# Kernel tuning notes

Measured on AMD Instinct MI355X. Metric: run time of the kernel, lower is better.

Reference implementation:

```python
import jax, jax.numpy as jnp
import numpy as np

S, L, D = 512, 128, 256        # sents, sent_len, embedding_dim (= out_hidden, skip_rnn)
V, E_V, E_D = 50000, 10000, 64  # vocab, entity vocab, entity dim
B, P = 128, 16                  # batch examples, positions per example
H2, F = D // 2, 256             # attn hidden, feature_size


def setup_inputs() -> dict:
    key = jax.random.key(0)
    ks = jax.random.split(key, 16)
    emb = jax.random.normal(ks[0], (V, D), jnp.float32) * 0.02
    emb = emb.at[0].set(0.0)  # padding_idx=0
    ent_emb = jax.random.normal(ks[1], (E_V, E_D), jnp.float32) * 0.02
    ent_emb = ent_emb.at[0].set(0.0)
    x = jax.random.randint(ks[2], (S, L), 0, V)
    ents = jax.random.randint(ks[3], (B, 2), 0, E_V)
    spos = jax.random.randint(ks[4], (B, P, 2), 0, L)  # valid for both sent(<S) and tok(<L) axes
    tpos = jax.random.randint(ks[5], (B, P, 2), 0, L)
    attw_W = jax.random.normal(ks[6], (H2, D), jnp.float32) / np.sqrt(D)
    attw_b = jnp.zeros((H2,), jnp.float32)
    attw2_W = jax.random.normal(ks[7], (1, H2), jnp.float32) / np.sqrt(H2)
    FEAT = 2 * D + 2 * E_D
    cond_W = jax.random.normal(ks[8], (F, FEAT), jnp.float32) / np.sqrt(FEAT)
    cond_b = jnp.zeros((F,), jnp.float32)
    lin_W = jax.random.normal(ks[9], (2, F), jnp.float32) / np.sqrt(F)
    lin_b = jnp.zeros((2,), jnp.float32)
    return {"x": x, "ents": ents, "spos": spos, "tpos": tpos,
            "emb": emb, "ent_emb": ent_emb,
            "attw_W": attw_W, "attw_b": attw_b, "attw2_W": attw2_W,
            "cond_W": cond_W, "cond_b": cond_b, "lin_W": lin_W, "lin_b": lin_b}


def _attn_pool(h, attw_W, attw_b, attw2_W):
    # h: [B, P, D]  ->  [B, D]
    energy = jnp.tanh(jnp.einsum('bpd,hd->bph', h, attw_W) + attw_b)
    logits = jnp.einsum('bph,oh->bpo', energy, attw2_W)[..., 0]   # [B, P]
    w = jax.nn.softmax(logits, axis=1)
    return jnp.einsum('bp,bpd->bd', w, h)


def reference(x, ents, spos, tpos, emb, ent_emb, attw_W, attw_b, attw2_W,
              cond_W, cond_b, lin_W, lin_b):
    sent_hiddens = emb[x]                                  # [S, L, D] (skip_rnn path)
    s_h = sent_hiddens[spos[..., 0], spos[..., 1]]         # [B, P, D] ragged gather (batched)
    t_h = sent_hiddens[tpos[..., 0], tpos[..., 1]]         # [B, P, D]
    s_pool = _attn_pool(s_h, attw_W, attw_b, attw2_W)      # [B, D]
    t_pool = _attn_pool(t_h, attw_W, attw_b, attw2_W)      # [B, D]
    e_embs = ent_emb[ents].reshape(ents.shape[0], -1)      # [B, 2*E_D]
    feats = jnp.concatenate([s_pool, t_pool, e_embs], axis=-1)  # [B, 2D+2E_D]
    condensed = feats @ cond_W.T + cond_b                  # [B, F]
    score = jnp.tanh(condensed) @ lin_W.T + lin_b          # [B, 2]
    return score
```

## Files before the change

kernel.cpp:

```cpp
#include <hip/hip_runtime.h>

#define S_ 512
#define L_ 128
#define D_ 256
#define B_ 128
#define P_ 16
#define H2_ 128
#define F_ 256
#define FEAT_ 640
#define ED_ 64
#define SH_STRIDE 264
#define LP_STRIDE 33

__global__ __launch_bounds__(512) void fused_kernel(
    const int* __restrict__ x, const int* __restrict__ ents,
    const int* __restrict__ spos, const int* __restrict__ tpos,
    const float* __restrict__ emb, const float* __restrict__ ent_emb,
    const float* __restrict__ attw_W, const float* __restrict__ attw_b,
    const float* __restrict__ attw2_W,
    const float* __restrict__ cond_W, const float* __restrict__ cond_b,
    const float* __restrict__ lin_W, const float* __restrict__ lin_b,
    float* __restrict__ out)
{
    const int b = blockIdx.x;
    const int t = threadIdx.x;
    const int pool = t >> 8;
    const int tl = t & 255;

    __shared__ float sh[2 * P_ * SH_STRIDE];
    __shared__ float lp[2 * P_ * LP_STRIDE];
    __shared__ float logits[32];
    __shared__ float wts[32];
    __shared__ float feats[FEAT_];
    __shared__ float part0[F_], part1[F_];
    __shared__ float r0s[4], r1s[4];

    const int pool_off = pool * P_ * SH_STRIDE;

    {
        const int* pos = pool ? tpos : spos;
        const int p = tl >> 4, i = tl & 15;
        const int si  = pos[(b * P_ + p) * 2 + 0];
        const int ti  = pos[(b * P_ + p) * 2 + 1];
        const int tok = x[si * L_ + ti];
        const float4* row = (const float4*)(emb + (size_t)tok * D_);
        float4* dst = (float4*)&sh[pool_off + p * SH_STRIDE + i * 16];
        #pragma unroll
        for (int j = 0; j < 4; ++j) dst[j] = row[i * 4 + j];
    }
    __syncthreads();

    {
        const int hp = tl >> 3, dh = tl & 7;
        const int h0 = hp * 4;
        const float4* W4 = (const float4*)attw_W;
        float bq0 = attw_b[h0],     bq1 = attw_b[h0 + 1];
        float bq2 = attw_b[h0 + 2], bq3 = attw_b[h0 + 3];
        float wq0 = attw2_W[h0],     wq1 = attw2_W[h0 + 1];
        float wq2 = attw2_W[h0 + 2], wq3 = attw2_W[h0 + 3];

        #pragma unroll
        for (int pass = 0; pass < 2; ++pass) {
            const int pb = pass * 8;
            float acc[4][8];
            #pragma unroll
            for (int q = 0; q < 4; ++q)
                #pragma unroll
                for (int p = 0; p < 8; ++p) acc[q][p] = 0.f;

            float4 nxt[4];
            #pragma unroll
            for (int q = 0; q < 4; ++q) nxt[q] = W4[(h0 + q) * 64 + dh];

            for (int c = 0; c < 8; ++c) {
                float4 a[4];
                #pragma unroll
                for (int q = 0; q < 4; ++q) a[q] = nxt[q];
                if (c < 7) {
                    #pragma unroll
                    for (int q = 0; q < 4; ++q)
                        nxt[q] = W4[(h0 + q) * 64 + 8 * (c + 1) + dh];
                }
                const int d = (8 * c + dh) * 4;
                #pragma unroll
                for (int p = 0; p < 8; ++p) {
                    float4 s = *(const float4*)&sh[pool_off + (pb + p) * SH_STRIDE + d];
                    #pragma unroll
                    for (int q = 0; q < 4; ++q)
                        acc[q][p] += a[q].x * s.x + a[q].y * s.y + a[q].z * s.z + a[q].w * s.w;
                }
            }

            #pragma unroll
            for (int q = 0; q < 4; ++q) {
                #pragma unroll
                for (int j = 0; j < 4; ++j) {
                    float lo = acc[q][j],     olo = __shfl_xor(lo, 4, 64);
                    float hi = acc[q][j + 4], ohi = __shfl_xor(hi, 4, 64);
                    acc[q][j] = (dh & 4) ? (hi + ohi) : (lo + olo);
                }
                #pragma unroll
                for (int j = 0; j < 2; ++j) {
                    float lo = acc[q][j],     olo = __shfl_xor(lo, 2, 64);
                    float hi = acc[q][j + 2], ohi = __shfl_xor(hi, 2, 64);
                    acc[q][j] = (dh & 2) ? (hi + ohi) : (lo + olo);
                }
                {
                    float lo = acc[q][0], olo = __shfl_xor(lo, 1, 64);
                    float hi = acc[q][1], ohi = __shfl_xor(hi, 1, 64);
                    acc[q][0] = (dh & 1) ? (hi + ohi) : (lo + olo);
                }
            }
            float v = tanhf(acc[0][0] + bq0) * wq0 + tanhf(acc[1][0] + bq1) * wq1
                    + tanhf(acc[2][0] + bq2) * wq2 + tanhf(acc[3][0] + bq3) * wq3;
            lp[pool * P_ * LP_STRIDE + (pb + dh) * LP_STRIDE + hp] = v;
        }
    }
    __syncthreads();

    {
        const int p = tl >> 4, g = tl & 15;
        const float* l = &lp[pool * P_ * LP_STRIDE + p * LP_STRIDE];
        float s = l[2 * g] + l[2 * g + 1];
        #pragma unroll
        for (int m = 1; m <= 8; m <<= 1) s += __shfl_xor(s, m, 64);
        if (g == 0) logits[pool * 16 + p] = s;
    }
    __syncthreads();

    if (tl < 16) {
        float l = logits[pool * 16 + tl];
        float m = l;
        for (int mm = 8; mm >= 1; mm >>= 1) m = fmaxf(m, __shfl_xor(m, mm, 64));
        float e = expf(l - m);
        float ssum = e;
        for (int mm = 8; mm >= 1; mm >>= 1) ssum += __shfl_xor(ssum, mm, 64);
        wts[pool * 16 + tl] = e / ssum;
    }
    __syncthreads();

    {
        float acc = 0.f;
        #pragma unroll
        for (int p = 0; p < P_; ++p)
            acc += wts[pool * 16 + p] * sh[pool_off + p * SH_STRIDE + tl];
        feats[pool * 256 + tl] = acc;
    }
    if (t < 128) {
        const int e = ents[b * 2 + (t >> 6)];
        feats[512 + t] = ent_emb[(size_t)e * ED_ + (t & 63)];
    }
    __syncthreads();

    {
        const int f = tl;
        const int cbase = pool ? 80 : 0;
        const float4* wrow = (const float4*)(cond_W + (size_t)f * FEAT_) + cbase;
        float acc = pool ? 0.f : cond_b[f];
        float4 buf[8];
        #pragma unroll
        for (int j = 0; j < 8; ++j) buf[j] = wrow[j];
        for (int c = 0; c < 80; c += 8) {
            float4 cur[8];
            #pragma unroll
            for (int j = 0; j < 8; ++j) cur[j] = buf[j];
            if (c + 8 < 80) {
                #pragma unroll
                for (int j = 0; j < 8; ++j) buf[j] = wrow[c + 8 + j];
            }
            #pragma unroll
            for (int j = 0; j < 8; ++j) {
                const float* fp = &feats[(cbase + c + j) * 4];
                acc += cur[j].x * fp[0] + cur[j].y * fp[1]
                     + cur[j].z * fp[2] + cur[j].w * fp[3];
            }
        }
        if (pool) part1[f] = acc; else part0[f] = acc;
    }
    __syncthreads();

    if (t < 256) {
        const float tv = tanhf(part0[t] + part1[t]);
        float v0 = tv * lin_W[t];
        float v1 = tv * lin_W[256 + t];
        #pragma unroll
        for (int m = 32; m >= 1; m >>= 1) {
            v0 += __shfl_xor(v0, m, 64);
            v1 += __shfl_xor(v1, m, 64);
        }
        if ((t & 63) == 0) { r0s[t >> 6] = v0; r1s[t >> 6] = v1; }
    }
    __syncthreads();
    if (t == 0) {
        out[b * 2 + 0] = r0s[0] + r0s[1] + r0s[2] + r0s[3] + lin_b[0];
        out[b * 2 + 1] = r1s[0] + r1s[1] + r1s[2] + r1s[3] + lin_b[1];
    }
}

extern "C" void kernel_launch(void* const* d_in, const int* in_sizes, int n_in,
                              void* d_out, int out_size, void* d_ws, size_t ws_size,
                              hipStream_t stream)
{
    const int* x     = (const int*)d_in[0];
    const int* ents  = (const int*)d_in[1];
    const int* spos  = (const int*)d_in[2];
    const int* tpos  = (const int*)d_in[3];
    const float* emb     = (const float*)d_in[4];
    const float* ent_emb = (const float*)d_in[5];
    const float* attw_W  = (const float*)d_in[6];
    const float* attw_b  = (const float*)d_in[7];
    const float* attw2_W = (const float*)d_in[8];
    const float* cond_W  = (const float*)d_in[9];
    const float* cond_b  = (const float*)d_in[10];
    const float* lin_W   = (const float*)d_in[11];
    const float* lin_b   = (const float*)d_in[12];
    float* out = (float*)d_out;

    fused_kernel<<<B_, 512, 0, stream>>>(
        x, ents, spos, tpos, emb, ent_emb, attw_W, attw_b, attw2_W,
        cond_W, cond_b, lin_W, lin_b, out);
}
```

Baseline: 138.0 us.

## Double block size to 1024 threads and restructure per-thread work split

Launches 1024 threads per block instead of 512. The gather now spreads each embedding row over 32 threads. The attention-energy loop is split so each thread handles one 8-position pass instead of two. The condensation GEMV is rewritten so 16 threads cooperate on one cond_W row, with coalesced float4 loads and a shuffle reduction, replacing one thread per row split in two halves. The aim is more parallelism and memory-level concurrency per block, since only 128 blocks run, at the cost of higher register pressure limits under launch_bounds(1024) and more idle threads in the serial phases.

```diff
diff --git a/kernel.cpp b/kernel.cpp
--- a/kernel.cpp
+++ b/kernel.cpp
@@ -12,7 +12,7 @@
 #define SH_STRIDE 264
 #define LP_STRIDE 33
 
-__global__ __launch_bounds__(512) void fused_kernel(
+__global__ __launch_bounds__(1024) void fused_kernel(
     const int* __restrict__ x, const int* __restrict__ ents,
     const int* __restrict__ spos, const int* __restrict__ tpos,
     const float* __restrict__ emb, const float* __restrict__ ent_emb,
@@ -24,102 +24,100 @@
 {
     const int b = blockIdx.x;
     const int t = threadIdx.x;
-    const int pool = t >> 8;
-    const int tl = t & 255;
 
     __shared__ float sh[2 * P_ * SH_STRIDE];
     __shared__ float lp[2 * P_ * LP_STRIDE];
     __shared__ float logits[32];
     __shared__ float wts[32];
     __shared__ float feats[FEAT_];
-    __shared__ float part0[F_], part1[F_];
+    __shared__ float part[F_];
     __shared__ float r0s[4], r1s[4];
 
-    const int pool_off = pool * P_ * SH_STRIDE;
-
     {
+        const int r = t >> 5, sub = t & 31;
+        const int pool = r >> 4, p = r & 15;
         const int* pos = pool ? tpos : spos;
-        const int p = tl >> 4, i = tl & 15;
         const int si  = pos[(b * P_ + p) * 2 + 0];
         const int ti  = pos[(b * P_ + p) * 2 + 1];
         const int tok = x[si * L_ + ti];
         const float4* row = (const float4*)(emb + (size_t)tok * D_);
-        float4* dst = (float4*)&sh[pool_off + p * SH_STRIDE + i * 16];
-        #pragma unroll
-        for (int j = 0; j < 4; ++j) dst[j] = row[i * 4 + j];
+        float* base = &sh[pool * P_ * SH_STRIDE + p * SH_STRIDE];
+        float4 v0 = row[sub];
+        float4 v1 = row[sub + 32];
+        *(float4*)&base[sub * 4]        = v0;
+        *(float4*)&base[128 + sub * 4]  = v1;
     }
     __syncthreads();
 
     {
+        const int q2 = t >> 8, tl = t & 255;
+        const int pool = q2 & 1, pb = (q2 >> 1) * 8;
+        const int pool_off = pool * P_ * SH_STRIDE;
         const int hp = tl >> 3, dh = tl & 7;
         const int h0 = hp * 4;
         const float4* W4 = (const float4*)attw_W;
-        float bq0 = attw_b[h0],     bq1 = attw_b[h0 + 1];
-        float bq2 = attw_b[h0 + 2], bq3 = attw_b[h0 + 3];
-        float wq0 = attw2_W[h0],     wq1 = attw2_W[h0 + 1];
-        float wq2 = attw2_W[h0 + 2], wq3 = attw2_W[h0 + 3];
-
-        #pragma unroll
-        for (int pass = 0; pass < 2; ++pass) {
-            const int pb = pass * 8;
-            float acc[4][8];
-            #pragma unroll
-            for (int q = 0; q < 4; ++q)
+
+        float acc[4][8];
+        #pragma unroll
+        for (int qq = 0; qq < 4; ++qq)
+            #pragma unroll
+            for (int p = 0; p < 8; ++p) acc[qq][p] = 0.f;
+
+        float4 nxt[4];
+        #pragma unroll
+        for (int qq = 0; qq < 4; ++qq) nxt[qq] = W4[(h0 + qq) * 64 + dh];
+
+        for (int c = 0; c < 8; ++c) {
+            float4 a[4];
+            #pragma unroll
+            for (int qq = 0; qq < 4; ++qq) a[qq] = nxt[qq];
+            if (c < 7) {
                 #pragma unroll
-                for (int p = 0; p < 8; ++p) acc[q][p] = 0.f;
-
-            float4 nxt[4];
-            #pragma unroll
-            for (int q = 0; q < 4; ++q) nxt[q] = W4[(h0 + q) * 64 + dh];
-
-            for (int c = 0; c < 8; ++c) {
-                float4 a[4];
+                for (int qq = 0; qq < 4; ++qq)
+                    nxt[qq] = W4[(h0 + qq) * 64 + 8 * (c + 1) + dh];
+            }
+            const int d = (8 * c + dh) * 4;
+            #pragma unroll
+            for (int p = 0; p < 8; ++p) {
+                float4 s = *(const float4*)&sh[pool_off + (pb + p) * SH_STRIDE + d];
                 #pragma unroll
-                for (int q = 0; q < 4; ++q) a[q] = nxt[q];
-                if (c < 7) {
-                    #pragma unroll
-                    for (int q = 0; q < 4; ++q)
-                        nxt[q] = W4[(h0 + q) * 64 + 8 * (c + 1) + dh];
-                }
-                const int d = (8 * c + dh) * 4;
-                #pragma unroll
-                for (int p = 0; p < 8; ++p) {
-                    float4 s = *(const float4*)&sh[pool_off + (pb + p) * SH_STRIDE + d];
-                    #pragma unroll
-                    for (int q = 0; q < 4; ++q)
-                        acc[q][p] += a[q].x * s.x + a[q].y * s.y + a[q].z * s.z + a[q].w * s.w;
-                }
-            }
-
-            #pragma unroll
-            for (int q = 0; q < 4; ++q) {
-                #pragma unroll
-                for (int j = 0; j < 4; ++j) {
-                    float lo = acc[q][j],     olo = __shfl_xor(lo, 4, 64);
-                    float hi = acc[q][j + 4], ohi = __shfl_xor(hi, 4, 64);
-                    acc[q][j] = (dh & 4) ? (hi + ohi) : (lo + olo);
-                }
-                #pragma unroll
-                for (int j = 0; j < 2; ++j) {
-                    float lo = acc[q][j],     olo = __shfl_xor(lo, 2, 64);
-                    float hi = acc[q][j + 2], ohi = __shfl_xor(hi, 2, 64);
-                    acc[q][j] = (dh & 2) ? (hi + ohi) : (lo + olo);
-                }
-                {
-                    float lo = acc[q][0], olo = __shfl_xor(lo, 1, 64);
-                    float hi = acc[q][1], ohi = __shfl_xor(hi, 1, 64);
-                    acc[q][0] = (dh & 1) ? (hi + ohi) : (lo + olo);
-                }
-            }
-            float v = tanhf(acc[0][0] + bq0) * wq0 + tanhf(acc[1][0] + bq1) * wq1
-                    + tanhf(acc[2][0] + bq2) * wq2 + tanhf(acc[3][0] + bq3) * wq3;
-            lp[pool * P_ * LP_STRIDE + (pb + dh) * LP_STRIDE + hp] = v;
-        }
-    }
-    __syncthreads();
-
-    {
-        const int p = tl >> 4, g = tl & 15;
+                for (int qq = 0; qq < 4; ++qq)
+                    acc[qq][p] += a[qq].x * s.x + a[qq].y * s.y + a[qq].z * s.z + a[qq].w * s.w;
+            }
+        }
+
+        #pragma unroll
+        for (int qq = 0; qq < 4; ++qq) {
+            #pragma unroll
+            for (int j = 0; j < 4; ++j) {
+                float lo = acc[qq][j],     olo = __shfl_xor(lo, 4, 64);
+                float hi = acc[qq][j + 4], ohi = __shfl_xor(hi, 4, 64);
+                acc[qq][j] = (dh & 4) ? (hi + ohi) : (lo + olo);
+            }
+            #pragma unroll
+            for (int j = 0; j < 2; ++j) {
+                float lo = acc[qq][j],     olo = __shfl_xor(lo, 2, 64);
+                float hi = acc[qq][j + 2], ohi = __shfl_xor(hi, 2, 64);
+                acc[qq][j] = (dh & 2) ? (hi + ohi) : (lo + olo);
+            }
+            {
+                float lo = acc[qq][0], olo = __shfl_xor(lo, 1, 64);
+                float hi = acc[qq][1], ohi = __shfl_xor(hi, 1, 64);
+                acc[qq][0] = (dh & 1) ? (hi + ohi) : (lo + olo);
+            }
+        }
+        const float b0 = attw_b[h0],     b1 = attw_b[h0 + 1];
+        const float b2 = attw_b[h0 + 2], b3 = attw_b[h0 + 3];
+        const float w0 = attw2_W[h0],     w1 = attw2_W[h0 + 1];
+        const float w2 = attw2_W[h0 + 2], w3 = attw2_W[h0 + 3];
+        float v = tanhf(acc[0][0] + b0) * w0 + tanhf(acc[1][0] + b1) * w1
+                + tanhf(acc[2][0] + b2) * w2 + tanhf(acc[3][0] + b3) * w3;
+        lp[pool * P_ * LP_STRIDE + (pb + dh) * LP_STRIDE + hp] = v;
+    }
+    __syncthreads();
+
+    if (t < 512) {
+        const int pool = t >> 8, p = (t >> 4) & 15, g = t & 15;
         const float* l = &lp[pool * P_ * LP_STRIDE + p * LP_STRIDE];
         float s = l[2 * g] + l[2 * g + 1];
         #pragma unroll
@@ -128,59 +126,56 @@
     }
     __syncthreads();
 
-    if (tl < 16) {
-        float l = logits[pool * 16 + tl];
+    if (t < 32) {
+        float l = logits[t];
         float m = l;
         for (int mm = 8; mm >= 1; mm >>= 1) m = fmaxf(m, __shfl_xor(m, mm, 64));
         float e = expf(l - m);
         float ssum = e;
         for (int mm = 8; mm >= 1; mm >>= 1) ssum += __shfl_xor(ssum, mm, 64);
-        wts[pool * 16 + tl] = e / ssum;
+        wts[t] = e / ssum;
+    }
+    __syncthreads();
+
+    if (t < 512) {
+        const int pool = t >> 8, d = t & 255;
+        const int pool_off = pool * P_ * SH_STRIDE;
+        float acc = 0.f;
+        #pragma unroll
+        for (int p = 0; p < P_; ++p)
+            acc += wts[pool * 16 + p] * sh[pool_off + p * SH_STRIDE + d];
+        feats[pool * 256 + d] = acc;
+    } else if (t < 640) {
+        const int i = t - 512;
+        const int e = ents[b * 2 + (i >> 6)];
+        feats[512 + i] = ent_emb[(size_t)e * ED_ + (i & 63)];
     }
     __syncthreads();
 
     {
-        float acc = 0.f;
-        #pragma unroll
-        for (int p = 0; p < P_; ++p)
-            acc += wts[pool * 16 + p] * sh[pool_off + p * SH_STRIDE + tl];
-        feats[pool * 256 + tl] = acc;
-    }
-    if (t < 128) {
-        const int e = ents[b * 2 + (t >> 6)];
-        feats[512 + t] = ent_emb[(size_t)e * ED_ + (t & 63)];
-    }
-    __syncthreads();
-
-    {
-        const int f = tl;
-        const int cbase = pool ? 80 : 0;
-        const float4* wrow = (const float4*)(cond_W + (size_t)f * FEAT_) + cbase;
-        float acc = pool ? 0.f : cond_b[f];
-        float4 buf[8];
-        #pragma unroll
-        for (int j = 0; j < 8; ++j) buf[j] = wrow[j];
-        for (int c = 0; c < 80; c += 8) {
-            float4 cur[8];
-            #pragma unroll
-            for (int j = 0; j < 8; ++j) cur[j] = buf[j];
-            if (c + 8 < 80) {
-                #pragma unroll
-                for (int j = 0; j < 8; ++j) buf[j] = wrow[c + 8 + j];
-            }
-            #pragma unroll
-            for (int j = 0; j < 8; ++j) {
-                const float* fp = &feats[(cbase + c + j) * 4];
-                acc += cur[j].x * fp[0] + cur[j].y * fp[1]
-                     + cur[j].z * fp[2] + cur[j].w * fp[3];
-            }
-        }
-        if (pool) part1[f] = acc; else part0[f] = acc;
+        const int g = t >> 4, sub = t & 15;
+        #pragma unroll
+        for (int k = 0; k < 4; ++k) {
+            const int r = g + 64 * k;
+            const float4* wrow = (const float4*)(cond_W + (size_t)r * FEAT_);
+            float4 w[10];
+            #pragma unroll
+            for (int j = 0; j < 10; ++j) w[j] = wrow[j * 16 + sub];
+            float acc = 0.f;
+            #pragma unroll
+            for (int j = 0; j < 10; ++j) {
+                const float* fp = &feats[(j * 16 + sub) * 4];
+                acc += w[j].x * fp[0] + w[j].y * fp[1] + w[j].z * fp[2] + w[j].w * fp[3];
+            }
+            #pragma unroll
+            for (int m = 1; m <= 8; m <<= 1) acc += __shfl_xor(acc, m, 64);
+            if (sub == 0) part[r] = acc + cond_b[r];
+        }
     }
     __syncthreads();
 
     if (t < 256) {
-        const float tv = tanhf(part0[t] + part1[t]);
+        const float tv = tanhf(part[t]);
         float v0 = tv * lin_W[t];
         float v1 = tv * lin_W[256 + t];
         #pragma unroll
@@ -216,7 +211,7 @@
     const float* lin_b   = (const float*)d_in[12];
     float* out = (float*)d_out;
 
-    fused_kernel<<<B_, 512, 0, stream>>>(
+    fused_kernel<<<B_, 1024, 0, stream>>>(
         x, ents, spos, tpos, emb, ent_emb, attw_W, attw_b, attw2_W,
         cond_W, cond_b, lin_W, lin_b, out);
 }
```

New measurement: 124.0 us. -10.2%, faster.
